# Optimization experiments

Measured on AMD Instinct MI355X. Metric: run time of the kernel, lower is better.

Reference implementation:

```python
import jax, jax.numpy as jnp
from jax import lax
import numpy as np

BETA = 0.5
ITERATION = 50
K = 1
EPS = 1e-5  # F.normalize eps


def cost_matrix_cosine(x, y):
    # x: [b,m,d], y: [b,n,d] -> cosine distance [b,m,n]
    xn = x / jnp.maximum(jnp.linalg.norm(x, axis=-1, keepdims=True), EPS)
    yn = y / jnp.maximum(jnp.linalg.norm(y, axis=-1, keepdims=True), EPS)
    return 1.0 - jnp.einsum('bmd,bnd->bmn', xn, yn)


def ipot(C, x_len, x_pad, y_len, y_pad, joint_pad, beta, iteration, k):
    # C: [b,m,n]; x_*: txt (m); y_*: img (n). Returns transport plan [b,m,n].
    b, m, n = C.shape
    jp_t = jnp.transpose(joint_pad, (0, 2, 1))                      # [b,n,m]
    A = jnp.where(jp_t, 0.0, jnp.exp(-jnp.transpose(C, (0, 2, 1)) / beta))
    T0 = jnp.where(jp_t, 0.0, 1.0)                                  # [b,n,m]
    sigma0 = jnp.where(x_pad, 0.0, 1.0 / x_len[:, None])[:, :, None]  # [b,m,1]
    x_mask = (x_pad.astype(C.dtype) * 1e4)[:, None, :]              # [b,1,m]
    y_mask = (y_pad.astype(C.dtype) * 1e4)[:, None, :]              # [b,1,n]
    xl = x_len[:, None, None]
    yl = y_len[:, None, None]

    def outer(carry, _):
        T, sigma = carry
        Q = A * T                                                   # [b,n,m]
        def inner(sig, _):
            # sig: [b,m,1]
            delta = 1.0 / (yl * jnp.transpose(jnp.matmul(Q, sig), (0, 2, 1)) + y_mask)  # [b,1,n]
            sig = jnp.transpose(1.0 / (xl * jnp.matmul(delta, Q) + x_mask), (0, 2, 1))  # [b,m,1]
            return sig, delta
        sigma, deltas = lax.scan(inner, sigma, None, length=k)
        delta = deltas[-1]                                          # [b,1,n]
        T = jnp.transpose(delta, (0, 2, 1)) * Q * jnp.transpose(sigma, (0, 2, 1))  # [b,n,m]
        return (T, sigma), None

    (T, _), _ = lax.scan(outer, (T0, sigma0), None, length=iteration)
    return jnp.transpose(T, (0, 2, 1))                              # [b,m,n]


def optimal_transport_dist(txt_emb, img_emb, txt_pad, img_pad):
    cost = cost_matrix_cosine(txt_emb, img_emb)                     # [b,m,n]
    joint_pad = txt_pad[:, :, None] | img_pad[:, None, :]           # [b,m,n]
    cost = jnp.where(joint_pad, 0.0, cost)
    txt_len = (txt_pad.shape[1] - jnp.sum(txt_pad, axis=1)).astype(cost.dtype)
    img_len = (img_pad.shape[1] - jnp.sum(img_pad, axis=1)).astype(cost.dtype)
    T = ipot(lax.stop_gradient(cost), txt_len, txt_pad, img_len, img_pad,
             joint_pad, BETA, ITERATION, K)
    # trace(cost @ T^T) == sum_ij cost_ij * plan_ij, per sample
    return jnp.sum(cost * lax.stop_gradient(T), axis=(1, 2))        # [b]


def reference(entitytxt_vec, object_vec, entitytxt_num, object_num):
    txt_nodes_emb = entitytxt_vec.astype(jnp.float32)               # [b,tl,d]
    img_nodes_emb = object_vec[:, 1:].astype(jnp.float32)           # [b,il,d]
    txt_pad = entitytxt_num == 0                                    # [b,tl] bool
    img_pad = object_num[:, 1:] == 0                                # [b,il] bool
    ot_dist = optimal_transport_dist(txt_nodes_emb, img_nodes_emb, txt_pad, img_pad)
    ot_loss = jnp.sum(ot_dist) * 0.01
    return ot_loss


def setup_inputs():
    key = jax.random.key(0)
    k1, k2, k3, k4 = jax.random.split(key, 4)
    b, tl, il1, d = 256, 128, 128, 1024
    entitytxt_vec = jax.random.normal(k1, (b, tl, d), dtype=jnp.float32)
    object_vec = jax.random.normal(k2, (b, il1, d), dtype=jnp.float32)
    entitytxt_num = jax.random.randint(k3, (b, tl), 0, 2, dtype=jnp.int32)
    object_num = jax.random.randint(k4, (b, il1), 0, 2, dtype=jnp.int32)
    # guarantee at least one valid node per sample (avoid 1/0 lengths)
    entitytxt_num = entitytxt_num.at[:, 0].set(1)
    object_num = object_num.at[:, 1].set(1)
    return {"entitytxt_vec": entitytxt_vec, "object_vec": object_vec,
            "entitytxt_num": entitytxt_num, "object_num": object_num}
```

## Files before the change

kernel.cpp:

```cpp
#include <hip/hip_runtime.h>
#include <math.h>

#define BATCH 256
#define M 128
#define NIMG 127
#define NP 128
#define D 1024
#define ITERS 50
#define ASTRIDE 132
#define NTHREADS 1024
#define NWAVES 16
#define NHALF 32

typedef __attribute__((ext_vector_type(8))) short bf16x8;
typedef __attribute__((ext_vector_type(4))) float floatx4;

static __device__ __forceinline__ unsigned pack_bf16x2(float a, float b) {
    unsigned ua = __builtin_bit_cast(unsigned, a);
    unsigned ub = __builtin_bit_cast(unsigned, b);
    ua += 0x7fffu + ((ua >> 16) & 1u);
    ub += 0x7fffu + ((ub >> 16) & 1u);
    return (ua >> 16) | (ub & 0xffff0000u);
}

static __device__ __forceinline__ bf16x8 pack8(const float4& a, const float4& b) {
    union { unsigned u[4]; bf16x8 v; } r;
    r.u[0] = pack_bf16x2(a.x, a.y);
    r.u[1] = pack_bf16x2(a.z, a.w);
    r.u[2] = pack_bf16x2(b.x, b.y);
    r.u[3] = pack_bf16x2(b.z, b.w);
    return r.v;
}

static __device__ __forceinline__ float sq8(const float4& a, const float4& b, float s) {
    s = fmaf(a.x, a.x, s); s = fmaf(a.y, a.y, s);
    s = fmaf(a.z, a.z, s); s = fmaf(a.w, a.w, s);
    s = fmaf(b.x, b.x, s); s = fmaf(b.y, b.y, s);
    s = fmaf(b.z, b.z, s); s = fmaf(b.w, b.w, s);
    return s;
}

template<int CTRL>
static __device__ __forceinline__ float dpp_add(float v) {
    int s = __builtin_amdgcn_update_dpp(0, __builtin_bit_cast(int, v), CTRL, 0xf, 0xf, true);
    return v + __builtin_bit_cast(float, s);
}
static __device__ __forceinline__ float red16(float v) {
    v = dpp_add<0x121>(v);
    v = dpp_add<0x122>(v);
    v = dpp_add<0x124>(v);
    v = dpp_add<0x128>(v);
    return v;
}

struct HalfBuf { float4 x0a, x0b, x1a, x1b, y0a, y0b, y1a, y1b; };

static __device__ __forceinline__ void load_half(HalfBuf& hb,
                                                 const float* __restrict__ xr0,
                                                 const float* __restrict__ xr1,
                                                 const float* __restrict__ yr0,
                                                 const float* __restrict__ yr1,
                                                 int h) {
    const int o = h * 32;
    hb.x0a = *(const float4*)(xr0 + o); hb.x0b = *(const float4*)(xr0 + o + 4);
    hb.x1a = *(const float4*)(xr1 + o); hb.x1b = *(const float4*)(xr1 + o + 4);
    hb.y0a = *(const float4*)(yr0 + o); hb.y0b = *(const float4*)(yr0 + o + 4);
    hb.y1a = *(const float4*)(yr1 + o); hb.y1b = *(const float4*)(yr1 + o + 4);
}

static __device__ __forceinline__ void proc_half(const HalfBuf& hb, bool yv0, bool yv1,
                                                 bool doX, bool doY,
                                                 floatx4 (&acc)[2][2],
                                                 float& ssx0, float& ssx1,
                                                 float& ssy0, float& ssy1) {
    const float4 z = make_float4(0.f, 0.f, 0.f, 0.f);
    float4 ya0 = yv0 ? hb.y0a : z, yb0 = yv0 ? hb.y0b : z;
    float4 ya1 = yv1 ? hb.y1a : z, yb1 = yv1 ? hb.y1b : z;

    if (doX) { ssx0 = sq8(hb.x0a, hb.x0b, ssx0); ssx1 = sq8(hb.x1a, hb.x1b, ssx1); }
    if (doY) { ssy0 = sq8(ya0, yb0, ssy0);       ssy1 = sq8(ya1, yb1, ssy1); }

    bf16x8 af0 = pack8(hb.x0a, hb.x0b);
    bf16x8 af1 = pack8(hb.x1a, hb.x1b);
    bf16x8 bf0 = pack8(ya0, yb0);
    bf16x8 bf1 = pack8(ya1, yb1);

    acc[0][0] = __builtin_amdgcn_mfma_f32_16x16x32_bf16(af0, bf0, acc[0][0], 0, 0, 0);
    acc[0][1] = __builtin_amdgcn_mfma_f32_16x16x32_bf16(af0, bf1, acc[0][1], 0, 0, 0);
    acc[1][0] = __builtin_amdgcn_mfma_f32_16x16x32_bf16(af1, bf0, acc[1][0], 0, 0, 0);
    acc[1][1] = __builtin_amdgcn_mfma_f32_16x16x32_bf16(af1, bf1, acc[1][1], 0, 0, 0);
}

__launch_bounds__(NTHREADS, 1)
__global__ void fused_kernel(const float* __restrict__ xg,
                             const float* __restrict__ yg,
                             const int* __restrict__ xnum,
                             const int* __restrict__ ynum,
                             float* __restrict__ out)
{
    __shared__ __align__(16) float Alds[M * ASTRIDE];
    __shared__ __align__(16) float partCS[NWAVES * 128];
    __shared__ __align__(16) float sdelta[NP];
    __shared__ __align__(16) float sxmask[M];
    __shared__ __align__(16) float symask[NP];
    __shared__ __align__(16) float sinvx[M];
    __shared__ __align__(16) float sinvy[NP];
    __shared__ float sxl_s, syl_s;
    __shared__ unsigned scnt[2 * NWAVES];
    __shared__ float swsum[NWAVES];

    const int b    = blockIdx.x;
    const int t    = threadIdx.x;
    const int lane = t & 63;
    const int w    = t >> 6;
    const int tj   = t & 15;
    const int i0   = (t >> 4) * 2;
    const int j0   = tj * 8;

    bool tpad = true, ipad = true;
    if (t < M)  { tpad = (xnum[b * M + t] == 0); sxmask[t] = tpad ? 1e4f : 0.0f; }
    if (t < NP) { ipad = !(t < NIMG && ynum[b * 128 + t + 1] != 0); symask[t] = ipad ? 1e4f : 0.0f; }
    unsigned long long bx = __ballot(t < M  && !tpad);
    unsigned long long by = __ballot(t < NP && !ipad);
    if (lane == 0) { scnt[w] = (unsigned)__popcll(bx); scnt[NWAVES + w] = (unsigned)__popcll(by); }
    __syncthreads();
    if (t == 0) {
        float xl = 0.f, yl = 0.f;
        for (int k = 0; k < NWAVES; ++k) { xl += scnt[k]; yl += scnt[NWAVES + k]; }
        sxl_s = xl; syl_s = yl;
    }

    const int wm = w & 3, wn = w >> 2;
    const int col = lane & 15, quad = lane >> 4;
    const int mbase = wm * 32, nbase = wn * 32;

    const float* xb = xg + (size_t)b * M * D;
    const float* yb = yg + ((size_t)b * 128 + 1) * D;

    const float* xr0 = xb + (size_t)(mbase + col) * D + quad * 8;
    const float* xr1 = xb + (size_t)(mbase + 16 + col) * D + quad * 8;
    const int yi0 = nbase + col, yi1 = nbase + 16 + col;
    const bool yv0 = (yi0 < NIMG), yv1 = (yi1 < NIMG);
    const float* yr0 = yb + (size_t)(yv0 ? yi0 : 0) * D + quad * 8;
    const float* yr1 = yb + (size_t)(yv1 ? yi1 : 0) * D + quad * 8;

    floatx4 acc[2][2];
#pragma unroll
    for (int a = 0; a < 2; ++a)
#pragma unroll
        for (int c = 0; c < 2; ++c) acc[a][c] = (floatx4)0.0f;

    float ssx0 = 0.f, ssx1 = 0.f, ssy0 = 0.f, ssy1 = 0.f;
    const bool doX = (wn == 0);
    const bool doY = (wm == 0);

    HalfBuf A, B;
    load_half(A, xr0, xr1, yr0, yr1, 0);
    load_half(B, xr0, xr1, yr0, yr1, 1);

#pragma unroll 1
    for (int hh = 0; hh < NHALF; hh += 2) {
        proc_half(A, yv0, yv1, doX, doY, acc, ssx0, ssx1, ssy0, ssy1);
        if (hh + 2 < NHALF) load_half(A, xr0, xr1, yr0, yr1, hh + 2);
        proc_half(B, yv0, yv1, doX, doY, acc, ssx0, ssx1, ssy0, ssy1);
        if (hh + 3 < NHALF) load_half(B, xr0, xr1, yr0, yr1, hh + 3);
        if ((hh & 6) == 6) __builtin_amdgcn_s_barrier();
    }

    if (doX) {
        float v0 = ssx0; v0 += __shfl_xor(v0, 16); v0 += __shfl_xor(v0, 32);
        float v1 = ssx1; v1 += __shfl_xor(v1, 16); v1 += __shfl_xor(v1, 32);
        if (quad == 0) {
            sinvx[mbase + col]      = 1.0f / fmaxf(sqrtf(v0), 1e-5f);
            sinvx[mbase + 16 + col] = 1.0f / fmaxf(sqrtf(v1), 1e-5f);
        }
    }
    if (doY) {
        float v0 = ssy0; v0 += __shfl_xor(v0, 16); v0 += __shfl_xor(v0, 32);
        float v1 = ssy1; v1 += __shfl_xor(v1, 16); v1 += __shfl_xor(v1, 32);
        if (quad == 0) {
            sinvy[nbase + col]      = 1.0f / fmaxf(sqrtf(v0), 1e-5f);
            sinvy[nbase + 16 + col] = 1.0f / fmaxf(sqrtf(v1), 1e-5f);
        }
    }
    __syncthreads();

#pragma unroll
    for (int tr = 0; tr < 2; ++tr)
#pragma unroll
        for (int tc = 0; tc < 2; ++tc) {
            const int n = nbase + tc * 16 + col;
            const float ivy_n = sinvy[n];
            const float ymf   = symask[n];
#pragma unroll
            for (int reg = 0; reg < 4; ++reg) {
                const int m = mbase + tr * 16 + quad * 4 + reg;
                const float p = acc[tr][tc][reg] * sinvx[m] * ivy_n;
                const float a = (sxmask[m] + ymf > 0.0f) ? 0.0f : expf(2.0f * p - 2.0f);
                Alds[m * ASTRIDE + n] = a;
            }
        }
    __syncthreads();

    const float xl = sxl_s, yl = syl_s;

    float xm[2], ym[8];
    xm[0] = sxmask[i0]; xm[1] = sxmask[i0 + 1];
    *(float4*)ym       = *(const float4*)(&symask[j0]);
    *(float4*)(ym + 4) = *(const float4*)(&symask[j0 + 4]);

    float sn[2];
#pragma unroll
    for (int r = 0; r < 2; ++r)
        sn[r] = (xm[r] > 0.0f) ? 0.0f : __builtin_amdgcn_rcpf(xl);

    float Af[2][8], Q[2][8];
#pragma unroll
    for (int r = 0; r < 2; ++r) {
        float4 a0 = *(const float4*)(&Alds[(i0 + r) * ASTRIDE + j0]);
        float4 a1 = *(const float4*)(&Alds[(i0 + r) * ASTRIDE + j0 + 4]);
        Af[r][0] = a0.x; Af[r][1] = a0.y; Af[r][2] = a0.z; Af[r][3] = a0.w;
        Af[r][4] = a1.x; Af[r][5] = a1.y; Af[r][6] = a1.z; Af[r][7] = a1.w;
#pragma unroll
        for (int j = 0; j < 8; ++j) Q[r][j] = Af[r][j];
    }
    __syncthreads();

    float lp = 0.0f;
    for (int itn = 0; itn < ITERS; ++itn) {
        float cp[8] = {0.f,0.f,0.f,0.f,0.f,0.f,0.f,0.f};
#pragma unroll
        for (int r = 0; r < 2; ++r)
#pragma unroll
            for (int j = 0; j < 8; ++j)
                cp[j] = fmaf(sn[r], Q[r][j], cp[j]);
#pragma unroll
        for (int j = 0; j < 8; ++j) {
            cp[j] += __shfl_xor(cp[j], 16);
            cp[j] += __shfl_xor(cp[j], 32);
        }
        if (lane < 16) {
            float4 c0 = make_float4(cp[0], cp[1], cp[2], cp[3]);
            float4 c1 = make_float4(cp[4], cp[5], cp[6], cp[7]);
            *(float4*)(&partCS[w * 128 + j0])     = c0;
            *(float4*)(&partCS[w * 128 + j0 + 4]) = c1;
        }
        __syncthreads();
        if (t < NP) {
            float s = 0.f;
#pragma unroll
            for (int w8 = 0; w8 < NWAVES; ++w8) s += partCS[w8 * 128 + t];
            sdelta[t] = __builtin_amdgcn_rcpf(yl * s + symask[t]);
        }
        __syncthreads();
        float dl[8];
        *(float4*)dl       = *(const float4*)(&sdelta[j0]);
        *(float4*)(dl + 4) = *(const float4*)(&sdelta[j0 + 4]);
        float rp[2] = {0.f, 0.f};
#pragma unroll
        for (int r = 0; r < 2; ++r)
#pragma unroll
            for (int j = 0; j < 8; ++j)
                rp[r] = fmaf(dl[j], Q[r][j], rp[r]);
#pragma unroll
        for (int r = 0; r < 2; ++r) rp[r] = red16(rp[r]);
#pragma unroll
        for (int r = 0; r < 2; ++r) rp[r] = __shfl(rp[r], lane & 48);
#pragma unroll
        for (int r = 0; r < 2; ++r)
            sn[r] = __builtin_amdgcn_rcpf(xl * rp[r] + xm[r]);

        if (itn < ITERS - 1) {
#pragma unroll
            for (int r = 0; r < 2; ++r) {
                const float f = sn[r];
#pragma unroll
                for (int j = 0; j < 8; ++j)
                    Q[r][j] *= Af[r][j] * dl[j] * f;
            }
        } else {
#pragma unroll
            for (int r = 0; r < 2; ++r)
#pragma unroll
                for (int j = 0; j < 8; ++j) {
                    const float a = Af[r][j];
                    if (a > 0.0f)
                        lp = fmaf(-0.5f * logf(a) * dl[j] * sn[r], Q[r][j], lp);
                }
        }
    }

#pragma unroll
    for (int off = 32; off > 0; off >>= 1) lp += __shfl_down(lp, off);
    if (lane == 0) swsum[w] = lp;
    __syncthreads();
    if (t == 0) {
        float tot = 0.f;
        for (int k = 0; k < NWAVES; ++k) tot += swsum[k];
        atomicAdd(out, 0.01f * tot);
    }
}

extern "C" void kernel_launch(void* const* d_in, const int* in_sizes, int n_in,
                              void* d_out, int out_size, void* d_ws, size_t ws_size,
                              hipStream_t stream) {
    const float* x  = (const float*)d_in[0];
    const float* y  = (const float*)d_in[1];
    const int*   xn = (const int*)d_in[2];
    const int*   yn = (const int*)d_in[3];
    float* out = (float*)d_out;
    (void)d_ws; (void)ws_size;

    (void)hipMemsetAsync(out, 0, (size_t)out_size * sizeof(float), stream);
    fused_kernel<<<dim3(BATCH), dim3(NTHREADS), 0, stream>>>(x, y, xn, yn, out);
}
```

Measured before the change: 423.2 us.

## Halve block to 512 threads with 32x64 MFMA tiles and 4 rows per thread

Reduces the fused kernel from 16 to 8 waves per block. Each wave now computes a 32x64 cost tile with eight MFMAs per step, and each thread holds four rows of the transport plan during the Sinkhorn-style iterations. The aim is cheaper barriers and a smaller cross-wave partial-sum reduction in the 50-iteration loop, plus more reuse of the loaded x fragments. In exchange register pressure roughly doubles, and each block has fewer waves to hide global-load latency in the GEMM phase.

```diff
diff --git a/kernel.cpp b/kernel.cpp
--- a/kernel.cpp
+++ b/kernel.cpp
@@ -8,8 +8,8 @@
 #define D 1024
 #define ITERS 50
 #define ASTRIDE 132
-#define NTHREADS 1024
-#define NWAVES 16
+#define NTHREADS 512
+#define NWAVES 8
 #define NHALF 32
 
 typedef __attribute__((ext_vector_type(8))) short bf16x8;
@@ -53,42 +53,63 @@
     return v;
 }
 
-struct HalfBuf { float4 x0a, x0b, x1a, x1b, y0a, y0b, y1a, y1b; };
+struct HalfBuf {
+    float4 x0a, x0b, x1a, x1b;
+    float4 y0a, y0b, y1a, y1b, y2a, y2b, y3a, y3b;
+};
 
 static __device__ __forceinline__ void load_half(HalfBuf& hb,
                                                  const float* __restrict__ xr0,
                                                  const float* __restrict__ xr1,
                                                  const float* __restrict__ yr0,
                                                  const float* __restrict__ yr1,
+                                                 const float* __restrict__ yr2,
+                                                 const float* __restrict__ yr3,
                                                  int h) {
     const int o = h * 32;
     hb.x0a = *(const float4*)(xr0 + o); hb.x0b = *(const float4*)(xr0 + o + 4);
     hb.x1a = *(const float4*)(xr1 + o); hb.x1b = *(const float4*)(xr1 + o + 4);
     hb.y0a = *(const float4*)(yr0 + o); hb.y0b = *(const float4*)(yr0 + o + 4);
     hb.y1a = *(const float4*)(yr1 + o); hb.y1b = *(const float4*)(yr1 + o + 4);
-}
-
-static __device__ __forceinline__ void proc_half(const HalfBuf& hb, bool yv0, bool yv1,
+    hb.y2a = *(const float4*)(yr2 + o); hb.y2b = *(const float4*)(yr2 + o + 4);
+    hb.y3a = *(const float4*)(yr3 + o); hb.y3b = *(const float4*)(yr3 + o + 4);
+}
+
+static __device__ __forceinline__ void proc_half(const HalfBuf& hb,
+                                                 bool yv0, bool yv1, bool yv2, bool yv3,
                                                  bool doX, bool doY,
-                                                 floatx4 (&acc)[2][2],
+                                                 floatx4 (&acc)[2][4],
                                                  float& ssx0, float& ssx1,
-                                                 float& ssy0, float& ssy1) {
+                                                 float (&ssy)[4]) {
     const float4 z = make_float4(0.f, 0.f, 0.f, 0.f);
-    float4 ya0 = yv0 ? hb.y0a : z, yb0 = yv0 ? hb.y0b : z;
-    float4 ya1 = yv1 ? hb.y1a : z, yb1 = yv1 ? hb.y1b : z;
+    float4 y0a = yv0 ? hb.y0a : z, y0b = yv0 ? hb.y0b : z;
+    float4 y1a = yv1 ? hb.y1a : z, y1b = yv1 ? hb.y1b : z;
+    float4 y2a = yv2 ? hb.y2a : z, y2b = yv2 ? hb.y2b : z;
+    float4 y3a = yv3 ? hb.y3a : z, y3b = yv3 ? hb.y3b : z;
 
     if (doX) { ssx0 = sq8(hb.x0a, hb.x0b, ssx0); ssx1 = sq8(hb.x1a, hb.x1b, ssx1); }
-    if (doY) { ssy0 = sq8(ya0, yb0, ssy0);       ssy1 = sq8(ya1, yb1, ssy1); }
+    if (doY) {
+        ssy[0] = sq8(y0a, y0b, ssy[0]);
+        ssy[1] = sq8(y1a, y1b, ssy[1]);
+        ssy[2] = sq8(y2a, y2b, ssy[2]);
+        ssy[3] = sq8(y3a, y3b, ssy[3]);
+    }
 
     bf16x8 af0 = pack8(hb.x0a, hb.x0b);
     bf16x8 af1 = pack8(hb.x1a, hb.x1b);
-    bf16x8 bf0 = pack8(ya0, yb0);
-    bf16x8 bf1 = pack8(ya1, yb1);
+    bf16x8 bf0 = pack8(y0a, y0b);
+    bf16x8 bf1 = pack8(y1a, y1b);
+    bf16x8 bf2 = pack8(y2a, y2b);
+    bf16x8 bf3 = pack8(y3a, y3b);
 
     acc[0][0] = __builtin_amdgcn_mfma_f32_16x16x32_bf16(af0, bf0, acc[0][0], 0, 0, 0);
     acc[0][1] = __builtin_amdgcn_mfma_f32_16x16x32_bf16(af0, bf1, acc[0][1], 0, 0, 0);
+    acc[0][2] = __builtin_amdgcn_mfma_f32_16x16x32_bf16(af0, bf2, acc[0][2], 0, 0, 0);
+    acc[0][3] = __builtin_amdgcn_mfma_f32_16x16x32_bf16(af0, bf3, acc[0][3], 0, 0, 0);
     acc[1][0] = __builtin_amdgcn_mfma_f32_16x16x32_bf16(af1, bf0, acc[1][0], 0, 0, 0);
     acc[1][1] = __builtin_amdgcn_mfma_f32_16x16x32_bf16(af1, bf1, acc[1][1], 0, 0, 0);
+    acc[1][2] = __builtin_amdgcn_mfma_f32_16x16x32_bf16(af1, bf2, acc[1][2], 0, 0, 0);
+    acc[1][3] = __builtin_amdgcn_mfma_f32_16x16x32_bf16(af1, bf3, acc[1][3], 0, 0, 0);
 }
 
 __launch_bounds__(NTHREADS, 1)
@@ -114,7 +135,7 @@
     const int lane = t & 63;
     const int w    = t >> 6;
     const int tj   = t & 15;
-    const int i0   = (t >> 4) * 2;
+    const int i0   = (t >> 4) * 4;
     const int j0   = tj * 8;
 
     bool tpad = true, ipad = true;
@@ -132,38 +153,43 @@
 
     const int wm = w & 3, wn = w >> 2;
     const int col = lane & 15, quad = lane >> 4;
-    const int mbase = wm * 32, nbase = wn * 32;
+    const int mbase = wm * 32, nbase = wn * 64;
 
     const float* xb = xg + (size_t)b * M * D;
     const float* yb = yg + ((size_t)b * 128 + 1) * D;
 
     const float* xr0 = xb + (size_t)(mbase + col) * D + quad * 8;
     const float* xr1 = xb + (size_t)(mbase + 16 + col) * D + quad * 8;
-    const int yi0 = nbase + col, yi1 = nbase + 16 + col;
+    const int yi0 = nbase + col,      yi1 = nbase + 16 + col;
+    const int yi2 = nbase + 32 + col, yi3 = nbase + 48 + col;
     const bool yv0 = (yi0 < NIMG), yv1 = (yi1 < NIMG);
+    const bool yv2 = (yi2 < NIMG), yv3 = (yi3 < NIMG);
     const float* yr0 = yb + (size_t)(yv0 ? yi0 : 0) * D + quad * 8;
     const float* yr1 = yb + (size_t)(yv1 ? yi1 : 0) * D + quad * 8;
-
-    floatx4 acc[2][2];
+    const float* yr2 = yb + (size_t)(yv2 ? yi2 : 0) * D + quad * 8;
+    const float* yr3 = yb + (size_t)(yv3 ? yi3 : 0) * D + quad * 8;
+
+    floatx4 acc[2][4];
 #pragma unroll
     for (int a = 0; a < 2; ++a)
 #pragma unroll
-        for (int c = 0; c < 2; ++c) acc[a][c] = (floatx4)0.0f;
-
-    float ssx0 = 0.f, ssx1 = 0.f, ssy0 = 0.f, ssy1 = 0.f;
+        for (int c = 0; c < 4; ++c) acc[a][c] = (floatx4)0.0f;
+
+    float ssx0 = 0.f, ssx1 = 0.f;
+    float ssy[4] = {0.f, 0.f, 0.f, 0.f};
     const bool doX = (wn == 0);
     const bool doY = (wm == 0);
 
     HalfBuf A, B;
-    load_half(A, xr0, xr1, yr0, yr1, 0);
-    load_half(B, xr0, xr1, yr0, yr1, 1);
+    load_half(A, xr0, xr1, yr0, yr1, yr2, yr3, 0);
+    load_half(B, xr0, xr1, yr0, yr1, yr2, yr3, 1);
 
 #pragma unroll 1
     for (int hh = 0; hh < NHALF; hh += 2) {
-        proc_half(A, yv0, yv1, doX, doY, acc, ssx0, ssx1, ssy0, ssy1);
-        if (hh + 2 < NHALF) load_half(A, xr0, xr1, yr0, yr1, hh + 2);
-        proc_half(B, yv0, yv1, doX, doY, acc, ssx0, ssx1, ssy0, ssy1);
-        if (hh + 3 < NHALF) load_half(B, xr0, xr1, yr0, yr1, hh + 3);
+        proc_half(A, yv0, yv1, yv2, yv3, doX, doY, acc, ssx0, ssx1, ssy);
+        if (hh + 2 < NHALF) load_half(A, xr0, xr1, yr0, yr1, yr2, yr3, hh + 2);
+        proc_half(B, yv0, yv1, yv2, yv3, doX, doY, acc, ssx0, ssx1, ssy);
+        if (hh + 3 < NHALF) load_half(B, xr0, xr1, yr0, yr1, yr2, yr3, hh + 3);
         if ((hh & 6) == 6) __builtin_amdgcn_s_barrier();
     }
 
@@ -176,11 +202,11 @@
         }
     }
     if (doY) {
-        float v0 = ssy0; v0 += __shfl_xor(v0, 16); v0 += __shfl_xor(v0, 32);
-        float v1 = ssy1; v1 += __shfl_xor(v1, 16); v1 += __shfl_xor(v1, 32);
-        if (quad == 0) {
-            sinvy[nbase + col]      = 1.0f / fmaxf(sqrtf(v0), 1e-5f);
-            sinvy[nbase + 16 + col] = 1.0f / fmaxf(sqrtf(v1), 1e-5f);
+#pragma unroll
+        for (int tc = 0; tc < 4; ++tc) {
+            float v = ssy[tc]; v += __shfl_xor(v, 16); v += __shfl_xor(v, 32);
+            if (quad == 0)
+                sinvy[nbase + tc * 16 + col] = 1.0f / fmaxf(sqrtf(v), 1e-5f);
         }
     }
     __syncthreads();
@@ -188,7 +214,7 @@
 #pragma unroll
     for (int tr = 0; tr < 2; ++tr)
 #pragma unroll
-        for (int tc = 0; tc < 2; ++tc) {
+        for (int tc = 0; tc < 4; ++tc) {
             const int n = nbase + tc * 16 + col;
             const float ivy_n = sinvy[n];
             const float ymf   = symask[n];
@@ -204,19 +230,19 @@
 
     const float xl = sxl_s, yl = syl_s;
 
-    float xm[2], ym[8];
-    xm[0] = sxmask[i0]; xm[1] = sxmask[i0 + 1];
+    float xm[4], ym[8];
+    *(float4*)xm       = *(const float4*)(&sxmask[i0]);
     *(float4*)ym       = *(const float4*)(&symask[j0]);
     *(float4*)(ym + 4) = *(const float4*)(&symask[j0 + 4]);
 
-    float sn[2];
-#pragma unroll
-    for (int r = 0; r < 2; ++r)
+    float sn[4];
+#pragma unroll
+    for (int r = 0; r < 4; ++r)
         sn[r] = (xm[r] > 0.0f) ? 0.0f : __builtin_amdgcn_rcpf(xl);
 
-    float Af[2][8], Q[2][8];
-#pragma unroll
-    for (int r = 0; r < 2; ++r) {
+    float Af[4][8], Q[4][8];
+#pragma unroll
+    for (int r = 0; r < 4; ++r) {
         float4 a0 = *(const float4*)(&Alds[(i0 + r) * ASTRIDE + j0]);
         float4 a1 = *(const float4*)(&Alds[(i0 + r) * ASTRIDE + j0 + 4]);
         Af[r][0] = a0.x; Af[r][1] = a0.y; Af[r][2] = a0.z; Af[r][3] = a0.w;
@@ -230,7 +256,7 @@
     for (int itn = 0; itn < ITERS; ++itn) {
         float cp[8] = {0.f,0.f,0.f,0.f,0.f,0.f,0.f,0.f};
 #pragma unroll
-        for (int r = 0; r < 2; ++r)
+        for (int r = 0; r < 4; ++r)
 #pragma unroll
             for (int j = 0; j < 8; ++j)
                 cp[j] = fmaf(sn[r], Q[r][j], cp[j]);
@@ -256,23 +282,23 @@
         float dl[8];
         *(float4*)dl       = *(const float4*)(&sdelta[j0]);
         *(float4*)(dl + 4) = *(const float4*)(&sdelta[j0 + 4]);
-        float rp[2] = {0.f, 0.f};
-#pragma unroll
-        for (int r = 0; r < 2; ++r)
+        float rp[4] = {0.f, 0.f, 0.f, 0.f};
+#pragma unroll
+        for (int r = 0; r < 4; ++r)
 #pragma unroll
             for (int j = 0; j < 8; ++j)
                 rp[r] = fmaf(dl[j], Q[r][j], rp[r]);
 #pragma unroll
-        for (int r = 0; r < 2; ++r) rp[r] = red16(rp[r]);
-#pragma unroll
-        for (int r = 0; r < 2; ++r) rp[r] = __shfl(rp[r], lane & 48);
-#pragma unroll
-        for (int r = 0; r < 2; ++r)
+        for (int r = 0; r < 4; ++r) rp[r] = red16(rp[r]);
+#pragma unroll
+        for (int r = 0; r < 4; ++r) rp[r] = __shfl(rp[r], lane & 48);
+#pragma unroll
+        for (int r = 0; r < 4; ++r)
             sn[r] = __builtin_amdgcn_rcpf(xl * rp[r] + xm[r]);
 
         if (itn < ITERS - 1) {
 #pragma unroll
-            for (int r = 0; r < 2; ++r) {
+            for (int r = 0; r < 4; ++r) {
                 const float f = sn[r];
 #pragma unroll
                 for (int j = 0; j < 8; ++j)
@@ -280,7 +306,7 @@
             }
         } else {
 #pragma unroll
-            for (int r = 0; r < 2; ++r)
+            for (int r = 0; r < 4; ++r)
 #pragma unroll
                 for (int j = 0; j < 8; ++j) {
                     const float a = Af[r][j];
```

New measurement: 353.9 us. -16.4%, faster.
